# Optimization experiments

Hardware: AMD Instinct MI355X
Metric: run time of the kernel (lower is better)

The kernel has to match this reference:

```python
import jax, jax.numpy as jnp
import numpy as np
from jax import lax

B, CIN, H, W = 2, 512, 64, 64
CD = CIN // 2            # down_dim = 256
CQ = CD // 8             # q/k channels = 32
EPS = 1e-5               # BatchNorm eps


def _conv3(x, w, b):
    # 3x3 conv, stride 1, padding 1 (init padding=1), NCHW/OIHW
    y = lax.conv_general_dilated(x, w, (1, 1), [(1, 1), (1, 1)],
                                 dimension_numbers=('NCHW', 'OIHW', 'NCHW'))
    return y + b[None, :, None, None]


def _bn(x, g, b, m, v):
    scale = g / jnp.sqrt(v + EPS)
    return x * scale[None, :, None, None] + (b - m * scale)[None, :, None, None]


def _prelu(x, a):
    return jnp.where(x > 0, x, a * x)


def _p1(x, w, b):
    # 1x1 conv as channel matmul
    return jnp.einsum('bchw,oc->bohw', x, w) + b[None, :, None, None]


def setup_inputs() -> dict:
    key = jax.random.key(0)
    it = iter(jax.random.split(key, 64))
    def nrm(shape, s=0.05):
        return jax.random.normal(next(it), shape, jnp.float32) * s
    inp = {
        'input_rgb': jax.random.normal(next(it), (B, CIN, H, W), jnp.float32),
        'input_dsm': jax.random.normal(next(it), (B, CIN, H, W), jnp.float32),
    }
    for m in ('rgb', 'dsm'):
        inp['conv_w_' + m] = nrm((CD, CIN, 3, 3))
        inp['conv_b_' + m] = nrm((CD,))
        inp['bn_g_' + m] = 1.0 + nrm((CD,))
        inp['bn_b_' + m] = nrm((CD,))
        inp['bn_m_' + m] = nrm((CD,))
        inp['bn_v_' + m] = jax.random.uniform(next(it), (CD,), jnp.float32, 0.5, 1.5)
        inp['prelu_' + m] = jnp.float32(0.25)
        inp['q_w_' + m] = nrm((CQ, CD)); inp['q_b_' + m] = nrm((CQ,))
        inp['k_w_' + m] = nrm((CQ, CD)); inp['k_b_' + m] = nrm((CQ,))
        inp['v_w_' + m] = nrm((CD, CD)); inp['v_b_' + m] = nrm((CD,))
        inp['up_w_' + m] = nrm((CIN, CD)); inp['up_b_' + m] = nrm((CIN,))
        inp['gamma_' + m] = jnp.float32(0.1)  # learned residual gate (zero-init in torch)
    return inp


def reference(input_rgb, input_dsm,
              conv_w_rgb, conv_b_rgb, bn_g_rgb, bn_b_rgb, bn_m_rgb, bn_v_rgb, prelu_rgb,
              q_w_rgb, q_b_rgb, k_w_rgb, k_b_rgb, v_w_rgb, v_b_rgb, up_w_rgb, up_b_rgb, gamma_rgb,
              conv_w_dsm, conv_b_dsm, bn_g_dsm, bn_b_dsm, bn_m_dsm, bn_v_dsm, prelu_dsm,
              q_w_dsm, q_b_dsm, k_w_dsm, k_b_dsm, v_w_dsm, v_b_dsm, up_w_dsm, up_b_dsm, gamma_dsm):
    conv_rgb = _prelu(_bn(_conv3(input_rgb, conv_w_rgb, conv_b_rgb),
                          bn_g_rgb, bn_b_rgb, bn_m_rgb, bn_v_rgb), prelu_rgb)
    conv_dsm = _prelu(_bn(_conv3(input_dsm, conv_w_dsm, conv_b_dsm),
                          bn_g_dsm, bn_b_dsm, bn_m_dsm, bn_v_dsm), prelu_dsm)
    b, c, h, w = conv_rgb.shape
    n = h * w
    q_rgb = _p1(conv_rgb, q_w_rgb, q_b_rgb).reshape(b, CQ, n)
    k_rgb = _p1(conv_rgb, k_w_rgb, k_b_rgb).reshape(b, CQ, n)
    v_rgb = _p1(conv_rgb, v_w_rgb, v_b_rgb).reshape(b, c, n)
    q_dsm = _p1(conv_dsm, q_w_dsm, q_b_dsm).reshape(b, CQ, n)
    k_dsm = _p1(conv_dsm, k_w_dsm, k_b_dsm).reshape(b, CQ, n)
    v_dsm = _p1(conv_dsm, v_w_dsm, v_b_dsm).reshape(b, c, n)
    # cross-modal unscaled attention: dsm queries attend over rgb keys
    attn_rgb = jax.nn.softmax(jnp.einsum('bqn,bqm->bnm', q_dsm, k_rgb), axis=-1)  # [b,n,n]
    o_rgb = jnp.einsum('bcj,bij->bci', v_rgb, attn_rgb).reshape(b, c, h, w)
    o_rgb = gamma_rgb * o_rgb + conv_rgb
    attn_dsm = jax.nn.softmax(jnp.einsum('bqn,bqm->bnm', q_rgb, k_dsm), axis=-1)
    o_dsm = jnp.einsum('bcj,bij->bci', v_dsm, attn_dsm).reshape(b, c, h, w)
    o_dsm = gamma_dsm * o_dsm + conv_dsm
    out_rgb = _p1(o_rgb, up_w_rgb, up_b_rgb) + input_rgb
    out_dsm = _p1(o_dsm, up_w_dsm, up_b_dsm) + input_dsm
    return (out_rgb, out_dsm)
```

## Files before the change

### kernel.cpp

```cpp
#include <hip/hip_runtime.h>
#include <hip/hip_bf16.h>
#include <stdint.h>


constexpr int CINCH = 512;
constexpr int NPIX  = 4096;

typedef __bf16 bf16x8 __attribute__((ext_vector_type(8)));
typedef __bf16 bf16x4 __attribute__((ext_vector_type(4)));
typedef float  f32x4  __attribute__((ext_vector_type(4)));

__device__ __forceinline__ __bf16 f2b(float f) {
    __hip_bfloat16 h = __float2bfloat16(f);
    return *reinterpret_cast<__bf16*>(&h);
}

__device__ __forceinline__ void load_lds16(const void* g, void* l) {
    __builtin_amdgcn_global_load_lds(
        (const __attribute__((address_space(1))) unsigned int*)(uintptr_t)g,
        (__attribute__((address_space(3))) unsigned int*)(uintptr_t)l,
        16, 0, 0);
}

__global__ __launch_bounds__(256)
void prep_w(const float* __restrict__ w_r, const float* __restrict__ w_d,
            const float* __restrict__ cb_r, const float* __restrict__ bg_r,
            const float* __restrict__ bb_r, const float* __restrict__ bm_r,
            const float* __restrict__ bv_r,
            const float* __restrict__ cb_d, const float* __restrict__ bg_d,
            const float* __restrict__ bb_d, const float* __restrict__ bm_d,
            const float* __restrict__ bv_d,
            __bf16* __restrict__ Wt, float* __restrict__ scA,
            float* __restrict__ shB, __bf16* __restrict__ zrow)
{
    const int t = threadIdx.x;
    const int blk = blockIdx.x;
    if (blk < 2304) {
        int gid = blk * 1024 + t * 4;
        int mod = gid >= 1179648;
        int o2  = gid - mod * 1179648;
        int tap = o2 >> 17;
        int r   = o2 & 131071;
        int oc  = r >> 9;
        int ic  = r & 511;
        const float* wsrc = mod ? w_d : w_r;
        long base = ((long)(oc * 512 + ic)) * 9 + tap;
        bf16x4 v;
        v.x = f2b(wsrc[base]);
        v.y = f2b(wsrc[base + 9]);
        v.z = f2b(wsrc[base + 18]);
        v.w = f2b(wsrc[base + 27]);
        *(bf16x4*)&Wt[gid] = v;
    } else if (blk == 2304) {
        unsigned short* z = (unsigned short*)zrow;
        z[t] = 0; z[t + 256] = 0;
    } else {
        int mod = blk - 2305;
        const float* cb = mod ? cb_d : cb_r;
        const float* bg = mod ? bg_d : bg_r;
        const float* bb = mod ? bb_d : bb_r;
        const float* bm = mod ? bm_d : bm_r;
        const float* bv = mod ? bv_d : bv_r;
        int oc = t;
        float sc = bg[oc] * rsqrtf(bv[oc] + 1e-5f);
        scA[mod * 256 + oc] = sc;
        shB[mod * 256 + oc] = (cb[oc] - bm[oc]) * sc + bb[oc];
    }
}

__global__ __launch_bounds__(256)
void prep_gw(const float* __restrict__ qw_r, const float* __restrict__ qw_d,
             const float* __restrict__ kw_r, const float* __restrict__ kw_d,
             const float* __restrict__ vw_r, const float* __restrict__ vw_d,
             const float* __restrict__ uw_r, const float* __restrict__ uw_d,
             __bf16* __restrict__ Wq, __bf16* __restrict__ Wk,
             __bf16* __restrict__ Wv, __bf16* __restrict__ Wu)
{
    int gid = blockIdx.x * 1024 + threadIdx.x * 4;
    __bf16* dst;
    float4 f = make_float4(0.f, 0.f, 0.f, 0.f);
    if (gid < 65536) {
        int mod = gid >> 15, e = gid & 32767;
        dst = Wq + gid;
        if (e < 8192) f = *(const float4*)((mod ? qw_d : qw_r) + e);
    } else if (gid < 131072) {
        int g = gid - 65536;
        int mod = g >> 15, e = g & 32767;
        dst = Wk + g;
        if (e < 8192) f = *(const float4*)((mod ? kw_d : kw_r) + e);
    } else if (gid < 262144) {
        int g = gid - 131072;
        int mod = g >> 16, e = g & 65535;
        dst = Wv + g;
        f = *(const float4*)((mod ? vw_d : vw_r) + e);
    } else {
        int g = gid - 262144;
        int mod = g >> 17, e = g & 131071;
        dst = Wu + g;
        f = *(const float4*)((mod ? uw_d : uw_r) + e);
    }
    bf16x4 o; o.x = f2b(f.x); o.y = f2b(f.y); o.z = f2b(f.z); o.w = f2b(f.w);
    *(bf16x4*)dst = o;
}

__global__ __launch_bounds__(256)
void xpose(const float* __restrict__ inr, const float* __restrict__ ind,
           __bf16* __restrict__ Xp)
{
    __shared__ float tile[32][33];
    const int t = threadIdx.x;
    const int p0 = blockIdx.x * 32;
    const int ic0 = blockIdx.y * 32;
    const int mb = blockIdx.z;
    const int mod = mb >> 1, b = mb & 1;
    const float* src = (mod ? ind : inr) + (long)b * CINCH * NPIX;

    int i = t >> 3, j4 = (t & 7) * 4;
    float4 v = *(const float4*)&src[(long)(ic0 + i) * NPIX + p0 + j4];
    tile[i][j4 + 0] = v.x; tile[i][j4 + 1] = v.y;
    tile[i][j4 + 2] = v.z; tile[i][j4 + 3] = v.w;
    __syncthreads();
    int j = t >> 3, i4 = (t & 7) * 4;
    bf16x4 o;
    o.x = f2b(tile[i4 + 0][j]);
    o.y = f2b(tile[i4 + 1][j]);
    o.z = f2b(tile[i4 + 2][j]);
    o.w = f2b(tile[i4 + 3][j]);
    *(bf16x4*)&Xp[((long)mb * NPIX + p0 + j) * 512 + ic0 + i4] = o;
}

__global__ __launch_bounds__(256)
void t256(const float* __restrict__ src, __bf16* __restrict__ dst)
{
    __shared__ float tile[32][33];
    const int t = threadIdx.x;
    const int p0 = blockIdx.x * 32;
    const int c0 = blockIdx.y * 32;
    const int mb = blockIdx.z;
    const float* s = src + (long)mb * 256 * NPIX;
    __bf16* d = dst + (long)mb * NPIX * 256;

    int i = t >> 3, j4 = (t & 7) * 4;
    float4 v = *(const float4*)&s[(long)(c0 + i) * NPIX + p0 + j4];
    tile[i][j4 + 0] = v.x; tile[i][j4 + 1] = v.y;
    tile[i][j4 + 2] = v.z; tile[i][j4 + 3] = v.w;
    __syncthreads();
    int j = t >> 3, i4 = (t & 7) * 4;
    bf16x4 o;
    o.x = f2b(tile[i4 + 0][j]); o.y = f2b(tile[i4 + 1][j]);
    o.z = f2b(tile[i4 + 2][j]); o.w = f2b(tile[i4 + 3][j]);
    *(bf16x4*)&d[((long)(p0 + j)) * 256 + c0 + i4] = o;
}

__global__ __launch_bounds__(256)
void conv_mfma(const __bf16* __restrict__ Wt, const __bf16* __restrict__ Xp,
               const __bf16* __restrict__ zrow, const float* __restrict__ scA,
               const float* __restrict__ shB, const float* __restrict__ prr,
               const float* __restrict__ prd, float* __restrict__ conv)
{
    __shared__ __bf16 As[64 * 32];
    __shared__ __bf16 Bs[128 * 32];

    const int t = threadIdx.x;
    const int n0 = blockIdx.x * 128;
    const int m0 = blockIdx.y * 64;
    const int mb = blockIdx.z;
    const int mod = mb >> 1;

    const __bf16* Am = Wt + (long)mod * 9 * 256 * 512;
    const __bf16* Xb = Xp + (long)mb * NPIX * 512;

    const int rowa = t >> 2;
    const int c16  = t & 3;
    char* ldsA  = (char*)As + (t >> 6) * 1024;
    char* ldsB0 = (char*)Bs + (t >> 6) * 1024;
    char* ldsB1 = ldsB0 + 4096;

    const int lane = t & 63, quad = lane >> 4, l15 = lane & 15, w = t >> 6;
    const int nw0 = w * 32;
    const char* abase = (const char*)As + l15 * 64 + quad * 16;
    const char* bbase = (const char*)Bs + (nw0 + l15) * 64 + quad * 16;

    f32x4 acc[4][2];
#pragma unroll
    for (int i = 0; i < 4; ++i)
#pragma unroll
        for (int j = 0; j < 2; ++j) acc[i][j] = (f32x4)0.f;

    for (int tap = 0; tap < 9; ++tap) {
        const int dy = tap / 3 - 1, dx = tap % 3 - 1;
        const __bf16* srcA = Am + (long)tap * 131072 + (long)(m0 + rowa) * 512 + c16 * 8;
        const __bf16* srcB0; const __bf16* srcB1;
        bool v0, v1;
        {
            int n = n0 + rowa;
            int x = n & 63, y = n >> 6;
            v0 = !((dx == -1 && x == 0) || (dx == 1 && x == 63) ||
                   (dy == -1 && y == 0) || (dy == 1 && y == 63));
            srcB0 = v0 ? (Xb + (long)(n + dy * 64 + dx) * 512 + c16 * 8)
                       : (zrow + c16 * 8);
            n += 64; x = n & 63; y = n >> 6;
            v1 = !((dx == -1 && x == 0) || (dx == 1 && x == 63) ||
                   (dy == -1 && y == 0) || (dy == 1 && y == 63));
            srcB1 = v1 ? (Xb + (long)(n + dy * 64 + dx) * 512 + c16 * 8)
                       : (zrow + c16 * 8);
        }

        for (int ic0 = 0; ic0 < 512; ic0 += 32) {
            load_lds16(srcA + ic0, ldsA);
            load_lds16(srcB0 + (v0 ? ic0 : 0), ldsB0);
            load_lds16(srcB1 + (v1 ? ic0 : 0), ldsB1);
            __syncthreads();

            bf16x8 af[4], bfr[2];
#pragma unroll
            for (int i = 0; i < 4; ++i) af[i]  = *(const bf16x8*)(abase + i * 1024);
#pragma unroll
            for (int j = 0; j < 2; ++j) bfr[j] = *(const bf16x8*)(bbase + j * 1024);
#pragma unroll
            for (int i = 0; i < 4; ++i)
#pragma unroll
                for (int j = 0; j < 2; ++j)
                    acc[i][j] = __builtin_amdgcn_mfma_f32_16x16x32_bf16(
                        af[i], bfr[j], acc[i][j], 0, 0, 0);
            __syncthreads();
        }
    }

    const float alpha = (mod ? prd : prr)[0];
    float* outp = conv + (long)mb * 256 * NPIX;
#pragma unroll
    for (int i = 0; i < 4; ++i) {
#pragma unroll
        for (int r = 0; r < 4; ++r) {
            int oc = m0 + 16 * i + quad * 4 + r;
            float sc = scA[mod * 256 + oc];
            float sh = shB[mod * 256 + oc];
            float* orow = outp + (long)oc * NPIX;
#pragma unroll
            for (int j = 0; j < 2; ++j) {
                int n = n0 + nw0 + 16 * j + l15;
                float y = acc[i][j][r] * sc + sh;
                y = (y > 0.f) ? y : alpha * y;
                orow[n] = y;
            }
        }
    }
}

__global__ __launch_bounds__(256)
void proj_mfma(const __bf16* __restrict__ Wb, int mstride,
               const __bf16* __restrict__ Bt,
               const float* __restrict__ bias_r, const float* __restrict__ bias_d,
               __bf16* __restrict__ dstT, __bf16* __restrict__ dstV,
               float* __restrict__ dstU,
               const float* __restrict__ resid_r, const float* __restrict__ resid_d,
               int mode, float oscale)
{
    __shared__ __bf16 As[128 * 32];
    __shared__ __bf16 Bs[128 * 32];

    const int t = threadIdx.x;
    const int n0 = blockIdx.x * 128;
    const int m0 = blockIdx.y * 128;
    const int mb = blockIdx.z;
    const int mod = mb >> 1, b = mb & 1;

    const __bf16* Am = Wb + (long)mod * mstride;
    const __bf16* Bm = Bt + (long)mb * (NPIX * 256);
    const float* bias = mod ? bias_d : bias_r;

    const int rowa = t >> 2, c16 = t & 3;
    char* ldsA0 = (char*)As + (t >> 6) * 1024;
    char* ldsA1 = ldsA0 + 4096;
    char* ldsB0 = (char*)Bs + (t >> 6) * 1024;
    char* ldsB1 = ldsB0 + 4096;
    const __bf16* srcA = Am + (long)(m0 + rowa) * 256 + c16 * 8;
    const __bf16* srcB = Bm + (long)(n0 + rowa) * 256 + c16 * 8;

    const int lane = t & 63, quad = lane >> 4, l15 = lane & 15, w = t >> 6;
    const int mw = (w >> 1) * 64, nw = (w & 1) * 64;
    const char* abase = (const char*)As + (mw + l15) * 64 + quad * 16;
    const char* bbase = (const char*)Bs + (nw + l15) * 64 + quad * 16;

    f32x4 acc[4][4];
#pragma unroll
    for (int i = 0; i < 4; ++i)
#pragma unroll
        for (int j = 0; j < 4; ++j) acc[i][j] = (f32x4)0.f;

    for (int kc = 0; kc < 256; kc += 32) {
        load_lds16(srcA + kc, ldsA0);
        load_lds16(srcA + kc + 16384, ldsA1);
        load_lds16(srcB + kc, ldsB0);
        load_lds16(srcB + kc + 16384, ldsB1);
        __syncthreads();

        bf16x8 af[4], bfr[4];
#pragma unroll
        for (int i = 0; i < 4; ++i) af[i]  = *(const bf16x8*)(abase + i * 1024);
#pragma unroll
        for (int j = 0; j < 4; ++j) bfr[j] = *(const bf16x8*)(bbase + j * 1024);
#pragma unroll
        for (int i = 0; i < 4; ++i)
#pragma unroll
            for (int j = 0; j < 4; ++j)
                acc[i][j] = __builtin_amdgcn_mfma_f32_16x16x32_bf16(
                    af[i], bfr[j], acc[i][j], 0, 0, 0);
        __syncthreads();
    }

    if (mode == 0) {
        if (mw == 0) {
            __bf16* dbase = dstT + (long)mb * (NPIX * 32);
#pragma unroll
            for (int fi = 0; fi < 2; ++fi)
#pragma unroll
                for (int r = 0; r < 4; ++r) {
                    int oc = 16 * fi + quad * 4 + r;
                    float bi = bias[oc];
#pragma unroll
                    for (int fj = 0; fj < 4; ++fj) {
                        int n = n0 + nw + 16 * fj + l15;
                        dbase[(long)n * 32 + oc] = f2b((acc[fi][fj][r] + bi) * oscale);
                    }
                }
        }
    } else if (mode == 1) {
        __bf16* dv = dstV + (long)mb * (256 * NPIX);
#pragma unroll
        for (int fi = 0; fi < 4; ++fi)
#pragma unroll
            for (int r = 0; r < 4; ++r) {
                int c = m0 + mw + 16 * fi + quad * 4 + r;
                float bi = bias[c];
                __bf16* row = dv + (long)c * NPIX;
#pragma unroll
                for (int fj = 0; fj < 4; ++fj) {
                    int n = n0 + nw + 16 * fj + l15;
                    row[n] = f2b(acc[fi][fj][r] + bi);
                }
            }
    } else {
        float* du = dstU + (long)mod * 4194304 + (long)b * 2097152;
        const float* rs = (mod ? resid_d : resid_r) + (long)b * 2097152;
#pragma unroll
        for (int fi = 0; fi < 4; ++fi)
#pragma unroll
            for (int r = 0; r < 4; ++r) {
                int oc = m0 + mw + 16 * fi + quad * 4 + r;
                float bi = bias[oc];
                const float* rrow = rs + (long)oc * NPIX;
                float* orow = du + (long)oc * NPIX;
#pragma unroll
                for (int fj = 0; fj < 4; ++fj) {
                    int n = n0 + nw + 16 * fj + l15;
                    orow[n] = acc[fi][fj][r] + bi + rrow[n];
                }
            }
    }
}

__global__ __launch_bounds__(256)
void attn_stats_mfma(const __bf16* __restrict__ Qt, const __bf16* __restrict__ Kt,
                     float* __restrict__ rmp, float* __restrict__ rlp)
{
    __shared__ __bf16 Qs[128 * 32];
    __shared__ __bf16 Ks[128 * 32];
    __shared__ float redm[2][128];
    __shared__ float redl[2][128];

    const int t  = threadIdx.x;
    const int i0 = blockIdx.x * 128;
    const int mbo = blockIdx.y;
    const int o  = mbo >> 1, b = mbo & 1;
    const int seg = blockIdx.z;
    const int jbase = seg * 1024;
    const int mbK = o * 2 + b, mbQ = (1 - o) * 2 + b;

    const __bf16* Qg = Qt + (long)mbQ * 131072;
    const __bf16* Kg = Kt + (long)mbK * 131072;

    const int lane = t & 63, quad = lane >> 4, l15 = lane & 15, w = t >> 6;
    const int mS = (w >> 1) * 64;
    const int nS = (w & 1) * 64;

    load_lds16((const char*)Qg + (long)i0 * 64 + t * 16, (char*)Qs + w * 1024);
    load_lds16((const char*)Qg + (long)i0 * 64 + 4096 + t * 16,
               (char*)Qs + 4096 + w * 1024);
    __syncthreads();

    bf16x8 qa[4];
#pragma unroll
    for (int fi = 0; fi < 4; ++fi)
        qa[fi] = *(const bf16x8*)((const char*)Qs + (mS + 16 * fi + l15) * 64 + quad * 16);

    const f32x4 zero4 = (f32x4)0.f;
    float m_t[16], l_t[16];
#pragma unroll
    for (int e = 0; e < 16; ++e) { m_t[e] = -3.0e38f; l_t[e] = 0.f; }

    for (int j0 = jbase; j0 < jbase + 1024; j0 += 128) {
        __syncthreads();
        load_lds16((const char*)Kg + (long)j0 * 64 + t * 16, (char*)Ks + w * 1024);
        load_lds16((const char*)Kg + (long)j0 * 64 + 4096 + t * 16,
                   (char*)Ks + 4096 + w * 1024);
        __syncthreads();

        bf16x8 kb[4];
#pragma unroll
        for (int fj = 0; fj < 4; ++fj)
            kb[fj] = *(const bf16x8*)((const char*)Ks + (nS + 16 * fj + l15) * 64 + quad * 16);
#pragma unroll
        for (int fi = 0; fi < 4; ++fi) {
            f32x4 sf[4];
#pragma unroll
            for (int fj = 0; fj < 4; ++fj)
                sf[fj] = __builtin_amdgcn_mfma_f32_16x16x32_bf16(qa[fi], kb[fj], zero4, 0, 0, 0);
#pragma unroll
            for (int r = 0; r < 4; ++r) {
                int e = fi * 4 + r;
                float a = fmaxf(fmaxf(sf[0][r], sf[1][r]), fmaxf(sf[2][r], sf[3][r]));
                float nm = fmaxf(m_t[e], a);
                float s = exp2f(sf[0][r] - nm) + exp2f(sf[1][r] - nm)
                        + exp2f(sf[2][r] - nm) + exp2f(sf[3][r] - nm);
                l_t[e] = l_t[e] * exp2f(m_t[e] - nm) + s;
                m_t[e] = nm;
            }
        }
    }

#pragma unroll
    for (int d = 1; d < 16; d <<= 1)
#pragma unroll
        for (int e = 0; e < 16; ++e) {
            float om = __shfl_xor(m_t[e], d, 64);
            float ol = __shfl_xor(l_t[e], d, 64);
            float nm = fmaxf(m_t[e], om);
            l_t[e] = l_t[e] * exp2f(m_t[e] - nm) + ol * exp2f(om - nm);
            m_t[e] = nm;
        }
    if (l15 == 0) {
#pragma unroll
        for (int fi = 0; fi < 4; ++fi)
#pragma unroll
            for (int r = 0; r < 4; ++r) {
                redm[w & 1][mS + 16 * fi + quad * 4 + r] = m_t[fi * 4 + r];
                redl[w & 1][mS + 16 * fi + quad * 4 + r] = l_t[fi * 4 + r];
            }
    }
    __syncthreads();
    if (t < 128) {
        float m0 = redm[0][t], m1 = redm[1][t];
        float l0 = redl[0][t], l1 = redl[1][t];
        float m = fmaxf(m0, m1);
        float l = l0 * exp2f(m0 - m) + l1 * exp2f(m1 - m);
        rmp[seg * 16384 + mbo * 4096 + i0 + t] = m;
        rlp[seg * 16384 + mbo * 4096 + i0 + t] = l;
    }
}

__global__ __launch_bounds__(256)
void stats_merge(const float* __restrict__ rmp, const float* __restrict__ rlp,
                 float* __restrict__ rmb, float* __restrict__ rlb)
{
    int idx = blockIdx.x * 256 + threadIdx.x;
    float m = rmp[idx];
#pragma unroll
    for (int s = 1; s < 4; ++s) m = fmaxf(m, rmp[s * 16384 + idx]);
    float l = 0.f;
#pragma unroll
    for (int s = 0; s < 4; ++s)
        l += rlp[s * 16384 + idx] * exp2f(rmp[s * 16384 + idx] - m);
    rmb[idx] = m;
    rlb[idx] = 1.f / l;
}

__global__ __launch_bounds__(256)
void attn_pv_mfma(const __bf16* __restrict__ Qt, const __bf16* __restrict__ Kt,
                  const __bf16* __restrict__ Vb,
                  float* __restrict__ part0, float* __restrict__ part1,
                  const float* __restrict__ rmb, const float* __restrict__ rlb)
{
    __shared__ __bf16 Qs[64 * 32];
    __shared__ __bf16 Ks[64 * 32];
    __shared__ __bf16 Vs[2 * 256 * 32];
    __shared__ __bf16 Ps[64 * 64];

    const int t  = threadIdx.x;
    const int i0 = blockIdx.x * 64;
    const int seg = blockIdx.y;
    const int mb = blockIdx.z;
    const int o  = mb >> 1, b = mb & 1;
    const int mbK = mb, mbQ = (1 - o) * 2 + b;
    const int jbase = seg * 2048;

    const __bf16* Qg = Qt + (long)mbQ * 131072;
    const __bf16* Kg = Kt + (long)mbK * 131072;
    const __bf16* Vg = Vb + (long)mbK * 1048576;
    const float* rm = rmb + mb * 4096;
    const float* rl = rlb + mb * 4096;

    const int lane = t & 63, quad = lane >> 4, l15 = lane & 15, w = t >> 6;
    const int iS = w * 16;
    const int cw = w * 64;

    load_lds16((const char*)Qg + (long)i0 * 64 + t * 16, (char*)Qs + w * 1024);

    float mlv[4], rlv[4];
#pragma unroll
    for (int r = 0; r < 4; ++r) mlv[r] = rm[i0 + iS + quad * 4 + r];
#pragma unroll
    for (int fj = 0; fj < 4; ++fj) rlv[fj] = rl[i0 + 16 * fj + l15];

    f32x4 acc[4][4];
#pragma unroll
    for (int i = 0; i < 4; ++i)
#pragma unroll
        for (int j = 0; j < 4; ++j) acc[i][j] = (f32x4)0.f;
    const f32x4 zero4 = (f32x4)0.f;

    __syncthreads();
    const bf16x8 qa = *(const bf16x8*)((const char*)Qs + (iS + l15) * 64 + quad * 16);

    const int clv = w * 16 + (lane >> 2);
    const int jb8 = (lane & 3) * 8;

    for (int j0 = jbase; j0 < jbase + 2048; j0 += 64) {
        __syncthreads();
        load_lds16((const char*)Kg + (long)j0 * 64 + t * 16, (char*)Ks + w * 1024);
        __syncthreads();

#pragma unroll
        for (int ii = 0; ii < 8; ++ii) {
            int ks = ii >> 2;
            int c = (ii & 3) * 64 + clv;
            load_lds16((const char*)Vg + (long)c * 8192 + (long)(j0 + ks * 32 + jb8) * 2,
                       (char*)Vs + ii * 4096 + w * 1024);
        }

        f32x4 sA[4];
#pragma unroll
        for (int fj = 0; fj < 4; ++fj) {
            bf16x8 kb = *(const bf16x8*)((const char*)Ks + (16 * fj + l15) * 64 + quad * 16);
            sA[fj] = __builtin_amdgcn_mfma_f32_16x16x32_bf16(qa, kb, zero4, 0, 0, 0);
        }
#pragma unroll
        for (int fj = 0; fj < 4; ++fj)
#pragma unroll
            for (int r = 0; r < 4; ++r) {
                int il = iS + quad * 4 + r;
                int boff = (il * 128 + (16 * fj + l15) * 2) ^ ((il & 12) << 3);
                *(__bf16*)((char*)Ps + boff) = f2b(exp2f(sA[fj][r] - mlv[r]));
            }
        __syncthreads();

#pragma unroll
        for (int ks = 0; ks < 2; ++ks) {
            bf16x8 va[4], pb[4];
#pragma unroll
            for (int fi = 0; fi < 4; ++fi)
                va[fi] = *(const bf16x8*)((const char*)Vs + ks * 16384 +
                                          (cw + 16 * fi + l15) * 64 + quad * 16);
#pragma unroll
            for (int fj = 0; fj < 4; ++fj) {
                int ip = 16 * fj + l15;
                int boff = (ip * 128 + ks * 64 + quad * 16) ^ ((ip & 12) << 3);
                pb[fj] = *(const bf16x8*)((const char*)Ps + boff);
            }
#pragma unroll
            for (int fi = 0; fi < 4; ++fi)
#pragma unroll
                for (int fj = 0; fj < 4; ++fj)
                    acc[fi][fj] = __builtin_amdgcn_mfma_f32_16x16x32_bf16(
                        va[fi], pb[fj], acc[fi][fj], 0, 0, 0);
        }
    }

    float* pg = (seg ? part1 : part0) + (long)mb * 1048576;
#pragma unroll
    for (int fi = 0; fi < 4; ++fi) {
#pragma unroll
        for (int r = 0; r < 4; ++r) {
            int c = cw + 16 * fi + quad * 4 + r;
            float* zr = pg + (long)c * 4096;
#pragma unroll
            for (int fj = 0; fj < 4; ++fj)
                zr[i0 + 16 * fj + l15] = acc[fi][fj][r] * rlv[fj];
        }
    }
}

__global__ __launch_bounds__(256)
void zred_t(const float* __restrict__ p0, const float* __restrict__ p1,
            const float* __restrict__ convb, __bf16* __restrict__ Zt,
            const float* __restrict__ g_r, const float* __restrict__ g_d)
{
    __shared__ float tile[32][33];
    const int t = threadIdx.x;
    const int pix0 = blockIdx.x * 32;
    const int c0 = blockIdx.y * 32;
    const int mb = blockIdx.z;
    const int o = mb >> 1;
    const float gamma = (o ? g_d : g_r)[0];
    const long base = (long)mb * 1048576;

    int i = t >> 3, j4 = (t & 7) * 4;
    long row = base + (long)(c0 + i) * 4096 + pix0 + j4;
    float4 a = *(const float4*)&p0[row];
    float4 b = *(const float4*)&p1[row];
    float4 cv = *(const float4*)&convb[row];
    tile[i][j4 + 0] = gamma * (a.x + b.x) + cv.x;
    tile[i][j4 + 1] = gamma * (a.y + b.y) + cv.y;
    tile[i][j4 + 2] = gamma * (a.z + b.z) + cv.z;
    tile[i][j4 + 3] = gamma * (a.w + b.w) + cv.w;
    __syncthreads();
    int j = t >> 3, i4 = (t & 7) * 4;
    bf16x4 oq;
    oq.x = f2b(tile[i4 + 0][j]); oq.y = f2b(tile[i4 + 1][j]);
    oq.z = f2b(tile[i4 + 2][j]); oq.w = f2b(tile[i4 + 3][j]);
    *(bf16x4*)&Zt[(long)mb * NPIX * 256 + (long)(pix0 + j) * 256 + c0 + i4] = oq;
}

extern "C" void kernel_launch(void* const* d_in, const int* in_sizes, int n_in,
                              void* d_out, int out_size, void* d_ws, size_t ws_size,
                              hipStream_t stream)
{
    const float* in_rgb = (const float*)d_in[0];
    const float* in_dsm = (const float*)d_in[1];
    auto P = [&](int i) { return (const float*)d_in[i]; };

    float* ws    = (float*)d_ws;
    float* conv  = ws;
    float* part0 = ws + 4194304;
    float* rmb   = ws + 8388608;
    float* rlb   = ws + 8404992;
    float* rmp   = part0;
    float* rlp   = part0 + 65536;
    float* scA   = ws + 8486912;
    float* shB   = ws + 8487424;
    __bf16* zrow = (__bf16*)(ws + 8487936);
    __bf16* Wt   = (__bf16*)(ws + 8488192);
    __bf16* Xp   = (__bf16*)(ws + 9667840);
    float*  part1 = ws + 9667840;
    __bf16* Qt   = (__bf16*)(ws + 13862144);
    __bf16* Kt   = (__bf16*)(ws + 14124288);
    __bf16* Vbb  = (__bf16*)(ws + 14386432);
    __bf16* Ct   = (__bf16*)(ws + 16483584);
    __bf16* Zt   = (__bf16*)(ws + 18580736);
    __bf16* Wq   = (__bf16*)(ws + 20677888);
    __bf16* Wk   = (__bf16*)(ws + 20710656);
    __bf16* Wv   = (__bf16*)(ws + 20743424);
    __bf16* Wu   = (__bf16*)(ws + 20808960);

    prep_w<<<2307, 256, 0, stream>>>(
        P(2), P(18), P(3), P(4), P(5), P(6), P(7),
        P(19), P(20), P(21), P(22), P(23),
        Wt, scA, shB, zrow);
    prep_gw<<<512, 256, 0, stream>>>(
        P(9), P(25), P(11), P(27), P(13), P(29), P(15), P(31),
        Wq, Wk, Wv, Wu);
    xpose<<<dim3(128, 16, 4), 256, 0, stream>>>(in_rgb, in_dsm, Xp);

    conv_mfma<<<dim3(32, 4, 4), 256, 0, stream>>>(
        Wt, Xp, zrow, scA, shB, P(8), P(24), conv);
    t256<<<dim3(128, 8, 4), 256, 0, stream>>>(conv, Ct);

    proj_mfma<<<dim3(32, 1, 4), 256, 0, stream>>>(
        Wq, 32768, Ct, P(10), P(26), Qt, nullptr, nullptr, nullptr, nullptr,
        0, 1.4426950408889634f);
    proj_mfma<<<dim3(32, 1, 4), 256, 0, stream>>>(
        Wk, 32768, Ct, P(12), P(28), Kt, nullptr, nullptr, nullptr, nullptr,
        0, 1.0f);
    proj_mfma<<<dim3(32, 2, 4), 256, 0, stream>>>(
        Wv, 65536, Ct, P(14), P(30), nullptr, Vbb, nullptr, nullptr, nullptr,
        1, 1.0f);

    attn_stats_mfma<<<dim3(32, 4, 4), 256, 0, stream>>>(Qt, Kt, rmp, rlp);
    stats_merge<<<64, 256, 0, stream>>>(rmp, rlp, rmb, rlb);

    attn_pv_mfma<<<dim3(64, 2, 4), 256, 0, stream>>>(
        Qt, Kt, Vbb, part0, part1, rmb, rlb);

    zred_t<<<dim3(128, 8, 4), 256, 0, stream>>>(
        part0, part1, conv, Zt, P(17), P(33));

    proj_mfma<<<dim3(32, 4, 4), 256, 0, stream>>>(
        Wu, 131072, Zt, P(16), P(32), nullptr, nullptr, (float*)d_out,
        in_rgb, in_dsm, 2, 1.0f);
}
```

Measured before the change: 385.9 us.

## Double-buffer conv_mfma LDS tiles with swizzled K=64 stages and 2 waves

Rewrites the implicit-GEMM conv kernel to use two waves per block, each computing a 64x64 output subtile. The K step is widened to 64 and LDS is double-buffered so the async global-to-LDS loads for the next step overlap with the MFMAs on the current one, roughly halving barriers. An XOR swizzle on LDS columns is added to avoid bank conflicts. Fewer threads per block means more loads per thread and fewer waves per CU for hiding latency.

```diff
diff --git a/kernel.cpp b/kernel.cpp
--- a/kernel.cpp
+++ b/kernel.cpp
@@ -152,14 +152,14 @@
     *(bf16x4*)&d[((long)(p0 + j)) * 256 + c0 + i4] = o;
 }
 
-__global__ __launch_bounds__(256)
+__global__ __launch_bounds__(128)
 void conv_mfma(const __bf16* __restrict__ Wt, const __bf16* __restrict__ Xp,
                const __bf16* __restrict__ zrow, const float* __restrict__ scA,
                const float* __restrict__ shB, const float* __restrict__ prr,
                const float* __restrict__ prd, float* __restrict__ conv)
 {
-    __shared__ __bf16 As[64 * 32];
-    __shared__ __bf16 Bs[128 * 32];
+    __shared__ __bf16 As[2 * 64 * 64];
+    __shared__ __bf16 Bs[2 * 128 * 64];
 
     const int t = threadIdx.x;
     const int n0 = blockIdx.x * 128;
@@ -167,64 +167,97 @@
     const int mb = blockIdx.z;
     const int mod = mb >> 1;
 
-    const __bf16* Am = Wt + (long)mod * 9 * 256 * 512;
+    const __bf16* Am = Wt + (long)mod * (9 * 256 * 512);
     const __bf16* Xb = Xp + (long)mb * NPIX * 512;
 
-    const int rowa = t >> 2;
-    const int c16  = t & 3;
-    char* ldsA  = (char*)As + (t >> 6) * 1024;
-    char* ldsB0 = (char*)Bs + (t >> 6) * 1024;
-    char* ldsB1 = ldsB0 + 4096;
-
-    const int lane = t & 63, quad = lane >> 4, l15 = lane & 15, w = t >> 6;
-    const int nw0 = w * 32;
-    const char* abase = (const char*)As + l15 * 64 + quad * 16;
-    const char* bbase = (const char*)Bs + (nw0 + l15) * 64 + quad * 16;
-
-    f32x4 acc[4][2];
+    const int w    = t >> 6;
+    const int srow = t >> 3;
+    const int cS   = (t & 7) ^ (srow & 7);
+    const __bf16* aBase = Am + (long)(m0 + srow) * 512 + cS * 8;
+    const __bf16* zsrc  = zrow + cS * 8;
+    const __bf16* bPtr0; const __bf16* bPtr1; const __bf16* bPtr2;
+    const __bf16* bPtr3; const __bf16* bPtr4; const __bf16* bPtr5;
+    const __bf16* bPtr6; const __bf16* bPtr7;
+    int bFlag[8];
+    {
+        const __bf16* bp[8];
+#pragma unroll
+        for (int c = 0; c < 8; ++c) {
+            int n = n0 + srow + 16 * c;
+            int x = n & 63, y = n >> 6;
+            bp[c] = Xb + (long)n * 512 + cS * 8;
+            bFlag[c] = (x == 0 ? 1 : 0) | (x == 63 ? 2 : 0) |
+                       (y == 0 ? 4 : 0) | (y == 63 ? 8 : 0);
+        }
+        bPtr0 = bp[0]; bPtr1 = bp[1]; bPtr2 = bp[2]; bPtr3 = bp[3];
+        bPtr4 = bp[4]; bPtr5 = bp[5]; bPtr6 = bp[6]; bPtr7 = bp[7];
+    }
+    char* ldsA = (char*)As + w * 1024;
+    char* ldsB = (char*)Bs + w * 1024;
+
+    const int lane = t & 63, quad = lane >> 4, l15 = lane & 15;
+    const int nw = w * 64;
+    const int soff0 = ((quad ^ (l15 & 7)) << 4);
+    const int soff1 = (((4 | quad) ^ (l15 & 7)) << 4);
+
+    f32x4 acc[4][4];
 #pragma unroll
     for (int i = 0; i < 4; ++i)
 #pragma unroll
-        for (int j = 0; j < 2; ++j) acc[i][j] = (f32x4)0.f;
-
-    for (int tap = 0; tap < 9; ++tap) {
+        for (int j = 0; j < 4; ++j) acc[i][j] = (f32x4)0.f;
+
+    auto stage = [&](int buf, int tap, int ic0) {
         const int dy = tap / 3 - 1, dx = tap % 3 - 1;
-        const __bf16* srcA = Am + (long)tap * 131072 + (long)(m0 + rowa) * 512 + c16 * 8;
-        const __bf16* srcB0; const __bf16* srcB1;
-        bool v0, v1;
-        {
-            int n = n0 + rowa;
-            int x = n & 63, y = n >> 6;
-            v0 = !((dx == -1 && x == 0) || (dx == 1 && x == 63) ||
-                   (dy == -1 && y == 0) || (dy == 1 && y == 63));
-            srcB0 = v0 ? (Xb + (long)(n + dy * 64 + dx) * 512 + c16 * 8)
-                       : (zrow + c16 * 8);
-            n += 64; x = n & 63; y = n >> 6;
-            v1 = !((dx == -1 && x == 0) || (dx == 1 && x == 63) ||
-                   (dy == -1 && y == 0) || (dy == 1 && y == 63));
-            srcB1 = v1 ? (Xb + (long)(n + dy * 64 + dx) * 512 + c16 * 8)
-                       : (zrow + c16 * 8);
-        }
-
-        for (int ic0 = 0; ic0 < 512; ic0 += 32) {
-            load_lds16(srcA + ic0, ldsA);
-            load_lds16(srcB0 + (v0 ? ic0 : 0), ldsB0);
-            load_lds16(srcB1 + (v1 ? ic0 : 0), ldsB1);
-            __syncthreads();
-
-            bf16x8 af[4], bfr[2];
-#pragma unroll
-            for (int i = 0; i < 4; ++i) af[i]  = *(const bf16x8*)(abase + i * 1024);
-#pragma unroll
-            for (int j = 0; j < 2; ++j) bfr[j] = *(const bf16x8*)(bbase + j * 1024);
+        const long doff = (long)(dy * 64 + dx) * 512 + ic0;
+        const __bf16* sa = aBase + (long)tap * 131072 + ic0;
+        char* la = ldsA + buf * 8192;
+        load_lds16(sa,         la);
+        load_lds16(sa + 8192,  la + 2048);
+        load_lds16(sa + 16384, la + 4096);
+        load_lds16(sa + 24576, la + 6144);
+        const int badmask = (dx == -1 ? 1 : 0) | (dx == 1 ? 2 : 0) |
+                            (dy == -1 ? 4 : 0) | (dy == 1 ? 8 : 0);
+        char* lb = ldsB + buf * 16384;
+        load_lds16((bFlag[0] & badmask) ? zsrc : (bPtr0 + doff), lb);
+        load_lds16((bFlag[1] & badmask) ? zsrc : (bPtr1 + doff), lb + 2048);
+        load_lds16((bFlag[2] & badmask) ? zsrc : (bPtr2 + doff), lb + 4096);
+        load_lds16((bFlag[3] & badmask) ? zsrc : (bPtr3 + doff), lb + 6144);
+        load_lds16((bFlag[4] & badmask) ? zsrc : (bPtr4 + doff), lb + 8192);
+        load_lds16((bFlag[5] & badmask) ? zsrc : (bPtr5 + doff), lb + 10240);
+        load_lds16((bFlag[6] & badmask) ? zsrc : (bPtr6 + doff), lb + 12288);
+        load_lds16((bFlag[7] & badmask) ? zsrc : (bPtr7 + doff), lb + 14336);
+    };
+
+    stage(0, 0, 0);
+    __syncthreads();
+
+    int cur = 0;
+    for (int step = 0; step < 72; ++step) {
+        if (step < 71) {
+            const int nxt = step + 1;
+            stage(cur ^ 1, nxt >> 3, (nxt & 7) << 6);
+        }
+        const char* ab = (const char*)As + cur * 8192;
+        const char* bb = (const char*)Bs + cur * 16384;
+#pragma unroll
+        for (int kk = 0; kk < 2; ++kk) {
+            const int so = kk ? soff1 : soff0;
+            bf16x8 af[4], bfr[4];
 #pragma unroll
             for (int i = 0; i < 4; ++i)
-#pragma unroll
-                for (int j = 0; j < 2; ++j)
+                af[i] = *(const bf16x8*)(ab + (16 * i + l15) * 128 + so);
+#pragma unroll
+            for (int j = 0; j < 4; ++j)
+                bfr[j] = *(const bf16x8*)(bb + (nw + 16 * j + l15) * 128 + so);
+#pragma unroll
+            for (int i = 0; i < 4; ++i)
+#pragma unroll
+                for (int j = 0; j < 4; ++j)
                     acc[i][j] = __builtin_amdgcn_mfma_f32_16x16x32_bf16(
                         af[i], bfr[j], acc[i][j], 0, 0, 0);
-            __syncthreads();
-        }
+        }
+        if (step < 71) __syncthreads();
+        cur ^= 1;
     }
 
     const float alpha = (mod ? prd : prr)[0];
@@ -238,8 +271,8 @@
             float sh = shB[mod * 256 + oc];
             float* orow = outp + (long)oc * NPIX;
 #pragma unroll
-            for (int j = 0; j < 2; ++j) {
-                int n = n0 + nw0 + 16 * j + l15;
+            for (int j = 0; j < 4; ++j) {
+                int n = n0 + nw + 16 * j + l15;
                 float y = acc[i][j][r] * sc + sh;
                 y = (y > 0.f) ? y : alpha * y;
                 orow[n] = y;
@@ -662,7 +695,7 @@
         Wq, Wk, Wv, Wu);
     xpose<<<dim3(128, 16, 4), 256, 0, stream>>>(in_rgb, in_dsm, Xp);
 
-    conv_mfma<<<dim3(32, 4, 4), 256, 0, stream>>>(
+    conv_mfma<<<dim3(32, 4, 4), 128, 0, stream>>>(
         Wt, Xp, zrow, scA, shB, P(8), P(24), conv);
     t256<<<dim3(128, 8, 4), 256, 0, stream>>>(conv, Ct);
 
```

Result: no change. 384.3 us (-0.4%).

## Restructure 3x3 conv to reuse halo-row input tiles across all nine taps

Applied to the files above, without the earlier changes.

The conv kernel now stages a 6-row halo of input pixels (64 channels at a time) into LDS once and reuses it for all nine taps, instead of reloading shifted input per tap. Weights are triple-buffered and the input tile double-buffered, using XOR-swizzled LDS layouts and explicit vmcnt waits to overlap global loads with MFMA. Each block now covers 4 output rows (256 pixels), so the grid is halved and each wave holds a larger accumulator tile. This cuts redundant global and LDS traffic for the conv but raises LDS use to about 120 KB per block, which lowers occupancy, and relies on hand-tuned wait counts being correct.

```diff
diff --git a/kernel.cpp b/kernel.cpp
--- a/kernel.cpp
+++ b/kernel.cpp
@@ -158,77 +158,116 @@
                const float* __restrict__ shB, const float* __restrict__ prr,
                const float* __restrict__ prd, float* __restrict__ conv)
 {
-    __shared__ __bf16 As[64 * 32];
-    __shared__ __bf16 Bs[128 * 32];
+    __shared__ __bf16 As[3 * 64 * 64];
+    __shared__ __bf16 Bs[2 * 385 * 64];
 
     const int t = threadIdx.x;
-    const int n0 = blockIdx.x * 128;
+    const int y0 = blockIdx.x * 4;
     const int m0 = blockIdx.y * 64;
     const int mb = blockIdx.z;
     const int mod = mb >> 1;
 
-    const __bf16* Am = Wt + (long)mod * 9 * 256 * 512;
+    const __bf16* Am = Wt + (long)mod * (9 * 256 * 512);
     const __bf16* Xb = Xp + (long)mb * NPIX * 512;
 
-    const int rowa = t >> 2;
-    const int c16  = t & 3;
-    char* ldsA  = (char*)As + (t >> 6) * 1024;
-    char* ldsB0 = (char*)Bs + (t >> 6) * 1024;
-    char* ldsB1 = ldsB0 + 4096;
-
     const int lane = t & 63, quad = lane >> 4, l15 = lane & 15, w = t >> 6;
-    const int nw0 = w * 32;
-    const char* abase = (const char*)As + l15 * 64 + quad * 16;
-    const char* bbase = (const char*)Bs + (nw0 + l15) * 64 + quad * 16;
-
-    f32x4 acc[4][2];
+
+    if (t < 16)
+        *(f32x4*)((char*)Bs + (t >> 3) * 49280 + 49152 + (t & 7) * 16) = (f32x4)0.f;
+    asm volatile("s_waitcnt lgkmcnt(0)" ::: "memory");
+
+    auto stage_a = [&](int buf, int tap, int cc) {
+#pragma unroll
+        for (int k = 0; k < 2; ++k) {
+            int r  = w * 16 + k * 8 + (lane >> 3);
+            int sl = (lane & 7) ^ (r & 7);
+            const __bf16* src = Am + (long)tap * 131072 + (long)(m0 + r) * 512
+                              + cc * 64 + sl * 8;
+            load_lds16(src, (char*)As + buf * 8192 + (w * 16 + k * 8) * 128);
+        }
+    };
+    auto stage_b = [&](int buf, int cc) {
+#pragma unroll
+        for (int k = 0; k < 12; ++k) {
+            int r  = w * 96 + k * 8 + (lane >> 3);
+            int sl = (lane & 7) ^ (r & 7);
+            int hr = r >> 6, xx = r & 63;
+            int gy = y0 + hr - 1;
+            const __bf16* src = ((unsigned)gy < 64u)
+                ? Xb + (long)(gy * 64 + xx) * 512 + cc * 64 + sl * 8
+                : zrow + sl * 8;
+            load_lds16(src, (char*)Bs + buf * 49280 + (w * 96 + k * 8) * 128);
+        }
+    };
+
+    f32x4 acc[4][4];
 #pragma unroll
     for (int i = 0; i < 4; ++i)
 #pragma unroll
-        for (int j = 0; j < 2; ++j) acc[i][j] = (f32x4)0.f;
-
-    for (int tap = 0; tap < 9; ++tap) {
-        const int dy = tap / 3 - 1, dx = tap % 3 - 1;
-        const __bf16* srcA = Am + (long)tap * 131072 + (long)(m0 + rowa) * 512 + c16 * 8;
-        const __bf16* srcB0; const __bf16* srcB1;
-        bool v0, v1;
-        {
-            int n = n0 + rowa;
-            int x = n & 63, y = n >> 6;
-            v0 = !((dx == -1 && x == 0) || (dx == 1 && x == 63) ||
-                   (dy == -1 && y == 0) || (dy == 1 && y == 63));
-            srcB0 = v0 ? (Xb + (long)(n + dy * 64 + dx) * 512 + c16 * 8)
-                       : (zrow + c16 * 8);
-            n += 64; x = n & 63; y = n >> 6;
-            v1 = !((dx == -1 && x == 0) || (dx == 1 && x == 63) ||
-                   (dy == -1 && y == 0) || (dy == 1 && y == 63));
-            srcB1 = v1 ? (Xb + (long)(n + dy * 64 + dx) * 512 + c16 * 8)
-                       : (zrow + c16 * 8);
-        }
-
-        for (int ic0 = 0; ic0 < 512; ic0 += 32) {
-            load_lds16(srcA + ic0, ldsA);
-            load_lds16(srcB0 + (v0 ? ic0 : 0), ldsB0);
-            load_lds16(srcB1 + (v1 ? ic0 : 0), ldsB1);
-            __syncthreads();
-
-            bf16x8 af[4], bfr[2];
-#pragma unroll
-            for (int i = 0; i < 4; ++i) af[i]  = *(const bf16x8*)(abase + i * 1024);
-#pragma unroll
-            for (int j = 0; j < 2; ++j) bfr[j] = *(const bf16x8*)(bbase + j * 1024);
-#pragma unroll
-            for (int i = 0; i < 4; ++i)
-#pragma unroll
-                for (int j = 0; j < 2; ++j)
-                    acc[i][j] = __builtin_amdgcn_mfma_f32_16x16x32_bf16(
-                        af[i], bfr[j], acc[i][j], 0, 0, 0);
-            __syncthreads();
+        for (int j = 0; j < 4; ++j) acc[i][j] = (f32x4)0.f;
+
+    stage_b(0, 0);
+    stage_a(0, 0, 0);
+    stage_a(1, 1, 0);
+
+    const int soffA0 = ((quad ^ (l15 & 7)) << 4);
+    const int soffA1 = (((4 | quad) ^ (l15 & 7)) << 4);
+
+    for (int c = 0; c < 8; ++c) {
+        for (int tp = 0; tp < 9; ++tp) {
+            const int s = c * 9 + tp;
+            if (s == 71)                  { asm volatile("s_waitcnt vmcnt(0)" ::: "memory"); }
+            else if (tp >= 7 && c < 7)    { asm volatile("s_waitcnt vmcnt(14)" ::: "memory"); }
+            else                          { asm volatile("s_waitcnt vmcnt(2)" ::: "memory"); }
+            __builtin_amdgcn_sched_barrier(0);
+            __builtin_amdgcn_s_barrier();
+            __builtin_amdgcn_sched_barrier(0);
+
+            if (s + 2 < 72) {
+                int c2 = (tp + 2 >= 9) ? c + 1 : c;
+                int t2 = (tp + 2 >= 9) ? tp - 7 : tp + 2;
+                int b2 = (s + 2) % 3;
+                stage_a(b2, t2, c2);
+            }
+            __builtin_amdgcn_sched_barrier(0);
+            if (tp == 6 && c < 7) stage_b((c + 1) & 1, c + 1);
+            __builtin_amdgcn_sched_barrier(0);
+
+            const char* ab = (const char*)As + (s % 3) * 8192;
+            const char* bb = (const char*)Bs + (c & 1) * 49280;
+            const int dy = tp / 3 - 1, dx = tp % 3 - 1;
+            const int hr = w + 1 + dy;
+            int rb[4];
+#pragma unroll
+            for (int fj = 0; fj < 4; ++fj) {
+                int x = fj * 16 + l15 + dx;
+                rb[fj] = ((unsigned)x < 64u) ? hr * 64 + x : 384;
+            }
+#pragma unroll
+            for (int kk = 0; kk < 2; ++kk) {
+                const int slq = kk * 4 + quad;
+                bf16x8 af[4], bfr[4];
+#pragma unroll
+                for (int i = 0; i < 4; ++i)
+                    af[i] = *(const bf16x8*)(ab + (16 * i + l15) * 128
+                                             + (kk ? soffA1 : soffA0));
+#pragma unroll
+                for (int fj = 0; fj < 4; ++fj)
+                    bfr[fj] = *(const bf16x8*)(bb + rb[fj] * 128
+                                               + ((slq ^ (rb[fj] & 7)) << 4));
+#pragma unroll
+                for (int i = 0; i < 4; ++i)
+#pragma unroll
+                    for (int fj = 0; fj < 4; ++fj)
+                        acc[i][fj] = __builtin_amdgcn_mfma_f32_16x16x32_bf16(
+                            af[i], bfr[fj], acc[i][fj], 0, 0, 0);
+            }
         }
     }
 
     const float alpha = (mod ? prd : prr)[0];
     float* outp = conv + (long)mb * 256 * NPIX;
+    const int nbase = (y0 + w) * 64;
 #pragma unroll
     for (int i = 0; i < 4; ++i) {
 #pragma unroll
@@ -238,9 +277,9 @@
             float sh = shB[mod * 256 + oc];
             float* orow = outp + (long)oc * NPIX;
 #pragma unroll
-            for (int j = 0; j < 2; ++j) {
-                int n = n0 + nw0 + 16 * j + l15;
-                float y = acc[i][j][r] * sc + sh;
+            for (int fj = 0; fj < 4; ++fj) {
+                int n = nbase + 16 * fj + l15;
+                float y = acc[i][fj][r] * sc + sh;
                 y = (y > 0.f) ? y : alpha * y;
                 orow[n] = y;
             }
@@ -662,7 +701,7 @@
         Wq, Wk, Wv, Wu);
     xpose<<<dim3(128, 16, 4), 256, 0, stream>>>(in_rgb, in_dsm, Xp);
 
-    conv_mfma<<<dim3(32, 4, 4), 256, 0, stream>>>(
+    conv_mfma<<<dim3(16, 4, 4), 256, 0, stream>>>(
         Wt, Xp, zrow, scA, shB, P(8), P(24), conv);
     t256<<<dim3(128, 8, 4), 256, 0, stream>>>(conv, Ct);
 
```

Result: faster. 367.0 us (-4.9%).
